# Kernel optimization log

Measured on AMD Instinct MI355X. Metric: run time of the kernel, lower is better.

## Reference

```python
import jax, jax.numpy as jnp
import numpy as np

B, H, W, C = 8, 64, 64, 384
HEADS, WS = 12, 14
KD = C // HEADS          # key_dim = 32
D = KD                    # attn_ratio = 1 -> d = key_dim
DH = D * HEADS            # = 384
HID = 4 * C               # mlp hidden = 1536
SCALE = KD ** -0.5
EPS = 1e-5
N = WS * WS               # 196 tokens per window


def _bias_idx():
    pts = [(i, j) for i in range(WS) for j in range(WS)]
    off, idxs = {}, []
    for p1 in pts:
        for p2 in pts:
            o = (abs(p1[0] - p2[0]), abs(p1[1] - p2[1]))
            if o not in off:
                off[o] = len(off)
            idxs.append(off[o])
    return np.asarray(idxs, np.int32).reshape(N, N), len(off)


def setup_inputs() -> dict:
    key = jax.random.key(0)
    ks = jax.random.split(key, 8)
    bias_idx_np, n_off = _bias_idx()  # n_off == 196 for a 14x14 window
    s = 0.02
    return {
        "x": jax.random.normal(ks[0], (B, H * W, C), jnp.float32),
        "ln_attn_w": jnp.ones((C,), jnp.float32),
        "ln_attn_b": jnp.zeros((C,), jnp.float32),
        "qkv_w": jax.random.normal(ks[1], (3 * DH, C), jnp.float32) * s,
        "qkv_b": jnp.zeros((3 * DH,), jnp.float32),
        "proj_w": jax.random.normal(ks[2], (C, DH), jnp.float32) * s,
        "proj_b": jnp.zeros((C,), jnp.float32),
        "attn_biases": jax.random.normal(ks[3], (HEADS, n_off), jnp.float32) * s,
        "conv_w": jax.random.normal(ks[4], (C, 1, 3, 3), jnp.float32) * s,  # depthwise OIHW
        "bn_w": jnp.ones((C,), jnp.float32),
        "bn_b": jnp.zeros((C,), jnp.float32),
        "bn_mean": jnp.zeros((C,), jnp.float32),
        "bn_var": jnp.ones((C,), jnp.float32),
        "ln_mlp_w": jnp.ones((C,), jnp.float32),
        "ln_mlp_b": jnp.zeros((C,), jnp.float32),
        "fc1_w": jax.random.normal(ks[5], (HID, C), jnp.float32) * s,
        "fc1_b": jnp.zeros((HID,), jnp.float32),
        "fc2_w": jax.random.normal(ks[6], (C, HID), jnp.float32) * s,
        "fc2_b": jnp.zeros((C,), jnp.float32),
        "bias_idx": jnp.asarray(bias_idx_np),
    }


def _ln(x, w, b):
    m = jnp.mean(x, -1, keepdims=True)
    v = jnp.mean((x - m) ** 2, -1, keepdims=True)
    return (x - m) * jax.lax.rsqrt(v + EPS) * w + b


def reference(x, ln_attn_w, ln_attn_b, qkv_w, qkv_b, proj_w, proj_b, attn_biases,
              conv_w, bn_w, bn_b, bn_mean, bn_var, ln_mlp_w, ln_mlp_b,
              fc1_w, fc1_b, fc2_w, fc2_b, bias_idx):
    L = H * W
    res = x
    # ---- window partition (pad 64 -> 70, 5x5 windows of 14x14) ----
    pad = (-H) % WS
    pH = H + pad
    n = pH // WS
    xw = x.reshape(B, H, W, C)
    xw = jnp.pad(xw, ((0, 0), (0, pad), (0, pad), (0, 0)))
    xw = xw.reshape(B, n, WS, n, WS, C).transpose(0, 1, 3, 2, 4, 5)
    xw = xw.reshape(B * n * n, N, C)
    # ---- attention with relative-position bias ----
    xn = _ln(xw, ln_attn_w, ln_attn_b)
    qkv = xn @ qkv_w.T + qkv_b                       # [Bw, N, 3*DH]
    qkv = qkv.reshape(-1, N, HEADS, 3 * KD)
    q, k, v = qkv[..., :KD], qkv[..., KD:2 * KD], qkv[..., 2 * KD:]
    bias = attn_biases[:, bias_idx]                  # [HEADS, N, N]
    attn = jnp.einsum('bnhd,bmhd->bhnm', q, k) * SCALE + bias[None]
    attn = jax.nn.softmax(attn, axis=-1)
    out = jnp.einsum('bhnm,bmhd->bnhd', attn, v).reshape(-1, N, DH)
    out = out @ proj_w.T + proj_b
    # ---- window reverse + crop + residual ----
    out = out.reshape(B, n, n, WS, WS, C).transpose(0, 1, 3, 2, 4, 5)
    out = out.reshape(B, pH, pH, C)[:, :H, :W]
    x = res + out.reshape(B, L, C)
    # ---- depthwise local conv + BN (eval mode) ----
    xc = x.reshape(B, H, W, C).transpose(0, 3, 1, 2)  # NCHW
    xc = jax.lax.conv_general_dilated(xc, conv_w, (1, 1), 'SAME',
                                      feature_group_count=C)
    inv = jax.lax.rsqrt(bn_var + 1e-5)
    xc = (xc - bn_mean[None, :, None, None]) * (inv * bn_w)[None, :, None, None] \
         + bn_b[None, :, None, None]
    x = xc.reshape(B, C, L).transpose(0, 2, 1)
    # ---- MLP (LN -> fc1 -> GELU(exact) -> fc2) + residual ----
    h = _ln(x, ln_mlp_w, ln_mlp_b)
    h = jax.nn.gelu(h @ fc1_w.T + fc1_b, approximate=False)
    h = h @ fc2_w.T + fc2_b
    return x + h
```

## Files before the change

### kernel.cpp

```cpp
#include <hip/hip_runtime.h>
#include <hip/hip_bf16.h>

#define DI __device__ __forceinline__

typedef __attribute__((ext_vector_type(8))) __bf16 bf16x8;
typedef __attribute__((ext_vector_type(4))) float f32x4;
typedef __attribute__((ext_vector_type(2))) float f32x2;
typedef __attribute__((ext_vector_type(8))) unsigned short us8;
typedef __attribute__((ext_vector_type(4))) unsigned short us4;

constexpr int CBATCH = 8;
constexpr int HW = 64;
constexpr int CDIM = 384;
constexpr int HEADS = 12;
constexpr int WS = 14;
constexpr int NTOK = 196;
constexpr int NWIN = 200;
constexpr int MV = 39200;
constexpr int MPAD = 39296;
constexpr int NQKV = 1152;
constexpr int HIDD = 1536;
constexpr int MMLP = 32768;
constexpr int NBIAS = 12 * 13 * 13 * 4 * 16 * 4;
constexpr int PLSTR = 228;
constexpr float SCALE = 0.17677669529663687f;

DI unsigned short f2bf(float f) { __bf16 b = (__bf16)f; return __builtin_bit_cast(unsigned short, b); }
DI float bf2f(unsigned short u) { unsigned x = (unsigned)u << 16; return __builtin_bit_cast(float, x); }
DI bf16x8 ldfrag(const unsigned short* p) { return __builtin_bit_cast(bf16x8, *(const us8*)p); }
DI f32x4 mfma16(bf16x8 a, bf16x8 b, f32x4 c) {
  return __builtin_amdgcn_mfma_f32_16x16x32_bf16(a, b, c, 0, 0, 0);
}
DI void async16(const void* g, void* l) {
  __builtin_amdgcn_global_load_lds((const __attribute__((address_space(1))) void*)g,
                                   (__attribute__((address_space(3))) void*)l, 16, 0, 0);
}
DI int vt_addr(int d, int t) {
  return d * 256 + (((t & ~7) ^ ((d & 7) << 3) ^ (((d >> 3) & 3) << 5)) | (t & 7));
}

__global__ __launch_bounds__(256) void k_cvt(const float* __restrict__ s,
                                             unsigned short* __restrict__ d, int n) {
  int i = blockIdx.x * 256 + threadIdx.x;
  if (i < n) d[i] = f2bf(s[i]);
}

__global__ __launch_bounds__(256) void k_bias2(const float* __restrict__ ab,
                                               const int* __restrict__ bidx,
                                               unsigned short* __restrict__ bt, int n_off) {
  int i = blockIdx.x * 256 + threadIdx.x;
  if (i >= NBIAS) return;
  int r = i & 3, l15 = (i >> 2) & 15, g = (i >> 6) & 3;
  int j = i >> 8;
  int kt = j % 13;
  int j2 = j / 13;
  int qt = j2 % 13;
  int h = j2 / 13;
  int q = qt * 16 + l15, k = kt * 16 + g * 4 + r;
  float v = 0.f;
  if (q < 196 && k < 196) v = ab[h * n_off + bidx[q * 196 + k]];
  bt[i] = f2bf(v);
}

template <int WIN>
__global__ __launch_bounds__(256) void k_ln(const float* __restrict__ src,
                                            const float* __restrict__ lw,
                                            const float* __restrict__ lb,
                                            unsigned short* __restrict__ dst) {
  const int row = blockIdx.x * 4 + (threadIdx.x >> 6);
  const int l = threadIdx.x & 63;
  const int c0 = l * 6;
  const float* p;
  bool valid;
  if (WIN) {
    int win = row / 196, t = row - win * 196;
    int b = win / 25, wi = win - b * 25;
    int wr = wi / 5, wc = wi - wr * 5;
    int hh = wr * 14 + t / 14, ww = wc * 14 + (t - (t / 14) * 14);
    valid = (row < MV) && (hh < HW) && (ww < HW);
    p = src + ((size_t)b * 4096 + hh * 64 + ww) * CDIM;
  } else {
    valid = true;
    p = src + (size_t)row * CDIM;
  }
  float v[6];
  if (valid) {
    f32x2 a = *(const f32x2*)(p + c0);
    f32x2 b2 = *(const f32x2*)(p + c0 + 2);
    f32x2 c2 = *(const f32x2*)(p + c0 + 4);
    v[0] = a.x; v[1] = a.y; v[2] = b2.x; v[3] = b2.y; v[4] = c2.x; v[5] = c2.y;
  } else {
#pragma unroll
    for (int k = 0; k < 6; ++k) v[k] = 0.f;
  }
  float s = 0.f, q = 0.f;
#pragma unroll
  for (int k = 0; k < 6; ++k) { s += v[k]; q += v[k] * v[k]; }
#pragma unroll
  for (int m = 1; m <= 32; m <<= 1) {
    s += __shfl_xor(s, m, 64);
    q += __shfl_xor(q, m, 64);
  }
  float mean = s * (1.0f / 384.0f);
  float var = q * (1.0f / 384.0f) - mean * mean;
  float rs = rsqrtf(var + 1e-5f);
#pragma unroll
  for (int k = 0; k < 6; ++k) {
    float y = (v[k] - mean) * rs * lw[c0 + k] + lb[c0 + k];
    dst[(size_t)row * CDIM + c0 + k] = f2bf(y);
  }
}

__global__ __launch_bounds__(256) void k_conv(const float* __restrict__ x1,
                                              const float* __restrict__ cw,
                                              const float* __restrict__ bw,
                                              const float* __restrict__ bb,
                                              const float* __restrict__ bm,
                                              const float* __restrict__ bv,
                                              float* __restrict__ x2) {
  int idx = blockIdx.x * 256 + threadIdx.x;
  int c = idx % 384;
  int x = (idx / 384) & 63;
  int b = idx / (384 * 64);
  const float* base = x1 + (size_t)b * 4096 * 384 + c;
  float w[9];
#pragma unroll
  for (int k = 0; k < 9; ++k) w[k] = cw[c * 9 + k];
  float sc = rsqrtf(bv[c] + 1e-5f) * bw[c];
  float sb = bb[c] - bm[c] * sc;
  float t0m = 0.f, t0c = 0.f, t0p = 0.f;
  float t1m, t1c, t1p, t2m, t2c, t2p;
  t1m = (x > 0) ? base[(x - 1) * 384] : 0.f;
  t1c = base[x * 384];
  t1p = (x < 63) ? base[(x + 1) * 384] : 0.f;
  for (int y = 0; y < 64; ++y) {
    if (y < 63) {
      int ro = (y + 1) * 64;
      t2m = (x > 0) ? base[(ro + x - 1) * 384] : 0.f;
      t2c = base[(ro + x) * 384];
      t2p = (x < 63) ? base[(ro + x + 1) * 384] : 0.f;
    } else { t2m = t2c = t2p = 0.f; }
    float o = w[0] * t0m + w[1] * t0c + w[2] * t0p +
              w[3] * t1m + w[4] * t1c + w[5] * t1p +
              w[6] * t2m + w[7] * t2c + w[8] * t2p;
    x2[((size_t)b * 4096 + y * 64 + x) * 384 + c] = o * sc + sb;
    t0m = t1m; t0c = t1c; t0p = t1p;
    t1m = t2m; t1c = t2c; t1p = t2p;
  }
}

__global__ __launch_bounds__(256, 3) void k_attn(const unsigned short* __restrict__ qkv,
                                                 const unsigned short* __restrict__ bias_t,
                                                 unsigned short* __restrict__ aout) {
  __shared__ unsigned short Vt[32 * 256];
  __shared__ unsigned short Pl[4][16 * PLSTR];
  const int bid = blockIdx.x;
  const int blk = (bid & 7) * 300 + (bid >> 3);
  const int win = blk / 12, h = blk - win * 12;
  const int tid = threadIdx.x;
  const int w = tid >> 6, l = tid & 63;
  const int l15 = l & 15, g = l >> 4;
  const unsigned short* qb = qkv + (size_t)win * 196 * 1152 + h * 96;

  for (int i = tid; i < 896; i += 256) {
    int t = i >> 2, d8 = (i & 3) << 3;
    us8 z = {0, 0, 0, 0, 0, 0, 0, 0};
    if (t < 196) z = *(const us8*)(qb + (size_t)t * 1152 + 64 + d8);
#pragma unroll
    for (int j = 0; j < 8; ++j) Vt[vt_addr(d8 + j, t)] = z[j];
  }
  for (int z = l; z < 16 * 20; z += 64) {
    int rr = z / 20, cc = 208 + (z - rr * 20);
    Pl[w][rr * PLSTR + cc] = 0;
  }
  __syncthreads();

  bf16x8 bkv[13];
#pragma unroll
  for (int kt = 0; kt < 13; ++kt)
    bkv[kt] = ldfrag(qb + (size_t)(kt * 16 + l15) * 1152 + 32 + g * 8);

  const unsigned short* bth = bias_t + (size_t)h * (13 * 13 * 4 * 16 * 4);
  unsigned short* plw = &Pl[w][0];
  for (int qt = w; qt < 13; qt += 4) {
    bf16x8 aq = ldfrag(qb + (size_t)(qt * 16 + l15) * 1152 + g * 8);
    us4 bv[13];
#pragma unroll
    for (int kt = 0; kt < 13; ++kt)
      bv[kt] = *(const us4*)(bth + (size_t)(((qt * 13 + kt) * 4 + g) * 16 + l15) * 4);

    float su = 0.f;
#pragma unroll
    for (int kt = 0; kt < 13; ++kt) {
      f32x4 zz = {0.f, 0.f, 0.f, 0.f};
      f32x4 s = mfma16(bkv[kt], aq, zz);
      us4 pk;
#pragma unroll
      for (int r = 0; r < 4; ++r) {
        float p = __expf(s[r] + bf2f(bv[kt][r]));
        if (kt == 12 && g != 0) p = 0.f;
        su += p;
        pk[r] = f2bf(p);
      }
      *(us4*)(plw + l15 * PLSTR + kt * 16 + g * 4) = pk;
    }
    su += __shfl_xor(su, 16, 64);
    su += __shfl_xor(su, 32, 64);
    asm volatile("s_waitcnt lgkmcnt(0)" ::: "memory");
    __builtin_amdgcn_sched_barrier(0);
    f32x4 o0 = {0.f, 0.f, 0.f, 0.f}, o1 = {0.f, 0.f, 0.f, 0.f};
#pragma unroll
    for (int kc = 0; kc < 7; ++kc) {
      int t0 = kc * 32 + g * 8;
      bf16x8 pa = ldfrag(plw + l15 * PLSTR + t0);
      bf16x8 b0 = ldfrag(&Vt[vt_addr(l15, t0)]);
      bf16x8 b1 = ldfrag(&Vt[vt_addr(16 + l15, t0)]);
      o0 = mfma16(pa, b0, o0);
      o1 = mfma16(pa, b1, o1);
    }
    float inv = 1.0f / su;
#pragma unroll
    for (int r = 0; r < 4; ++r) {
      int rw = qt * 16 + g * 4 + r;
      if (rw < 196) {
        size_t rb = ((size_t)win * 196 + rw) * 384 + h * 32;
        aout[rb + l15] = f2bf(o0[r] * inv);
        aout[rb + 16 + l15] = f2bf(o1[r] * inv);
      }
    }
  }
}

template <int MODE, int K>
__global__ __launch_bounds__(256) void k_gemm(const unsigned short* __restrict__ A,
                                              const unsigned short* __restrict__ B,
                                              const float* __restrict__ bias,
                                              const float* __restrict__ auxr,
                                              float* __restrict__ auxw,
                                              unsigned short* __restrict__ outb) {
  __shared__ unsigned short As[128 * 64];
  __shared__ unsigned short Bs[128 * 64];
  const int tid = threadIdx.x;
  const int w = tid >> 6, l = tid & 63;
  const int l15 = l & 15, g = l >> 4;
  const int wm = w >> 1, wn = w & 1;
  const int nwg = gridDim.x * gridDim.y;
  const int orig = blockIdx.y * gridDim.x + blockIdx.x;
  const int cq = nwg >> 3, cr = nwg & 7;
  const int xcd = orig & 7, cidx = orig >> 3;
  const int flat = (xcd < cr ? xcd * (cq + 1) : cr * (cq + 1) + (xcd - cr) * cq) + cidx;
  const int bx = flat % gridDim.x, by = flat / gridDim.x;
  const size_t arow0 = (size_t)bx * 128;
  const size_t brow0 = (size_t)by * 128;
  f32x4 acc[4][4] = {};
  for (int ks = 0; ks < K; ks += 64) {
    if (ks) __syncthreads();
#pragma unroll
    for (int it = 0; it < 4; ++it) {
      const int f = it * 256 + tid;
      const int r = f >> 3, c8 = (f & 7) << 3;
      const int c8s = c8 ^ ((r & 7) << 3);
      const int lb = (it * 256 + w * 64) * 8;
      async16(A + (arow0 + r) * K + ks + c8s, &As[lb]);
      async16(B + (brow0 + r) * K + ks + c8s, &Bs[lb]);
    }
    __syncthreads();
#pragma unroll
    for (int kk = 0; kk < 2; ++kk) {
      bf16x8 af[4], bfr[4];
#pragma unroll
      for (int i = 0; i < 4; ++i) {
        const int row = wm * 64 + i * 16 + l15;
        af[i] = ldfrag(&As[row * 64 + ((kk * 32 + g * 8) ^ ((row & 7) << 3))]);
      }
#pragma unroll
      for (int j = 0; j < 4; ++j) {
        const int row = wn * 64 + j * 16 + l15;
        bfr[j] = ldfrag(&Bs[row * 64 + ((kk * 32 + g * 8) ^ ((row & 7) << 3))]);
      }
#pragma unroll
      for (int i = 0; i < 4; ++i)
#pragma unroll
        for (int j = 0; j < 4; ++j)
          acc[i][j] = mfma16(af[i], bfr[j], acc[i][j]);
    }
  }
#pragma unroll
  for (int i = 0; i < 4; ++i) {
#pragma unroll
    for (int j = 0; j < 4; ++j) {
#pragma unroll
      for (int r = 0; r < 4; ++r) {
        const int row = (int)arow0 + wm * 64 + i * 16 + g * 4 + r;
        const int col = (int)brow0 + wn * 64 + j * 16 + l15;
        float v = acc[i][j][r] + bias[col];
        if (MODE == 0) {
          int ch = col % 96;
          float o = (ch < 32) ? v * SCALE : v;
          outb[(size_t)row * NQKV + col] = f2bf(o);
        } else if (MODE == 1) {
          if (row < MV) {
            int win = row / 196, t = row - win * 196;
            int b = win / 25, wi = win - b * 25;
            int wr = wi / 5, wc = wi - wr * 5;
            int hh = wr * 14 + t / 14, ww = wc * 14 + (t - (t / 14) * 14);
            if (hh < HW && ww < HW) {
              size_t di = ((size_t)b * 4096 + hh * 64 + ww) * 384 + col;
              auxw[di] = auxr[di] + v;
            }
          }
        } else if (MODE == 2) {
          float gl = 0.5f * v * (1.0f + erff(v * 0.7071067811865475f));
          outb[(size_t)row * HIDD + col] = f2bf(gl);
        } else {
          size_t di = (size_t)row * 384 + col;
          auxw[di] = auxr[di] + v;
        }
      }
    }
  }
}

extern "C" void kernel_launch(void* const* d_in, const int* in_sizes, int n_in,
                              void* d_out, int out_size, void* d_ws, size_t ws_size,
                              hipStream_t stream) {
  const float* x = (const float*)d_in[0];
  const float* ln_attn_w = (const float*)d_in[1];
  const float* ln_attn_b = (const float*)d_in[2];
  const float* qkv_w = (const float*)d_in[3];
  const float* qkv_b = (const float*)d_in[4];
  const float* proj_w = (const float*)d_in[5];
  const float* proj_b = (const float*)d_in[6];
  const float* attn_biases = (const float*)d_in[7];
  const float* conv_w = (const float*)d_in[8];
  const float* bn_w = (const float*)d_in[9];
  const float* bn_b = (const float*)d_in[10];
  const float* bn_mean = (const float*)d_in[11];
  const float* bn_var = (const float*)d_in[12];
  const float* ln_mlp_w = (const float*)d_in[13];
  const float* ln_mlp_b = (const float*)d_in[14];
  const float* fc1_w = (const float*)d_in[15];
  const float* fc1_b = (const float*)d_in[16];
  const float* fc2_w = (const float*)d_in[17];
  const float* fc2_b = (const float*)d_in[18];
  const int* bias_idx = (const int*)d_in[19];

  char* ws = (char*)d_ws;
  size_t off = 0;
  auto alloc = [&](size_t n) {
    void* p = ws + off;
    off = (off + n + 255) & ~(size_t)255;
    return p;
  };
  unsigned short* xn = (unsigned short*)alloc((size_t)MPAD * CDIM * 2);
  unsigned short* qkv = (unsigned short*)alloc((size_t)MMLP * HIDD * 2);
  unsigned short* attn = (unsigned short*)alloc((size_t)MMLP * CDIM * 4);
  float* x1 = (float*)alloc((size_t)MMLP * CDIM * 4);
  unsigned short* wq = (unsigned short*)alloc((size_t)NQKV * CDIM * 2);
  unsigned short* wp = (unsigned short*)alloc((size_t)CDIM * CDIM * 2);
  unsigned short* w1 = (unsigned short*)alloc((size_t)HIDD * CDIM * 2);
  unsigned short* w2 = (unsigned short*)alloc((size_t)CDIM * HIDD * 2);
  unsigned short* bias_t = (unsigned short*)alloc((size_t)NBIAS * 2);
  unsigned short* hbuf = qkv;
  float* x2 = (float*)attn;
  unsigned short* xln = xn;
  int n_off = in_sizes[7] / HEADS;

  dim3 B256(256);
  k_cvt<<<dim3((NQKV * CDIM + 255) / 256), B256, 0, stream>>>(qkv_w, wq, NQKV * CDIM);
  k_cvt<<<dim3((CDIM * CDIM + 255) / 256), B256, 0, stream>>>(proj_w, wp, CDIM * CDIM);
  k_cvt<<<dim3((HIDD * CDIM + 255) / 256), B256, 0, stream>>>(fc1_w, w1, HIDD * CDIM);
  k_cvt<<<dim3((CDIM * HIDD + 255) / 256), B256, 0, stream>>>(fc2_w, w2, CDIM * HIDD);
  k_bias2<<<dim3((NBIAS + 255) / 256), B256, 0, stream>>>(attn_biases, bias_idx, bias_t, n_off);
  k_ln<1><<<dim3(MPAD / 4), B256, 0, stream>>>(x, ln_attn_w, ln_attn_b, xn);
  k_gemm<0, CDIM><<<dim3(MPAD / 128, NQKV / 128), B256, 0, stream>>>(xn, wq, qkv_b, nullptr, nullptr, qkv);
  k_attn<<<dim3(NWIN * HEADS), B256, 0, stream>>>(qkv, bias_t, attn);
  k_gemm<1, CDIM><<<dim3(MPAD / 128, CDIM / 128), B256, 0, stream>>>(attn, wp, proj_b, x, x1, nullptr);
  k_conv<<<dim3(CBATCH * HW * CDIM / 256), B256, 0, stream>>>(x1, conv_w, bn_w, bn_b, bn_mean, bn_var, x2);
  k_ln<0><<<dim3(MMLP / 4), B256, 0, stream>>>(x2, ln_mlp_w, ln_mlp_b, xln);
  k_gemm<2, CDIM><<<dim3(MMLP / 128, HIDD / 128), B256, 0, stream>>>(xln, w1, fc1_b, nullptr, nullptr, hbuf);
  k_gemm<3, HIDD><<<dim3(MMLP / 128, CDIM / 128), B256, 0, stream>>>(hbuf, w2, fc2_b, x2, (float*)d_out, nullptr);
}
```

Baseline: 557.5 us.

## Double-buffer LDS tiles in GEMM to overlap async loads with MFMA

Shared-memory A/B tiles in the GEMM kernel become two buffers. The next K-slice is issued asynchronously into one buffer while MFMAs consume the other, with the loop unrolled by two K-steps. This is meant to hide global-to-LDS load latency and cut one barrier per K-step. It doubles LDS use per block to 64KB, which can lower occupancy, and the loop assumes an even number of K tiles.

```diff
diff --git a/kernel.cpp b/kernel.cpp
--- a/kernel.cpp
+++ b/kernel.cpp
@@ -238,8 +238,8 @@
                                               const float* __restrict__ auxr,
                                               float* __restrict__ auxw,
                                               unsigned short* __restrict__ outb) {
-  __shared__ unsigned short As[128 * 64];
-  __shared__ unsigned short Bs[128 * 64];
+  __shared__ unsigned short As[2][128 * 64];
+  __shared__ unsigned short Bs[2][128 * 64];
   const int tid = threadIdx.x;
   const int w = tid >> 6, l = tid & 63;
   const int l15 = l & 15, g = l >> 4;
@@ -253,30 +253,31 @@
   const size_t arow0 = (size_t)bx * 128;
   const size_t brow0 = (size_t)by * 128;
   f32x4 acc[4][4] = {};
-  for (int ks = 0; ks < K; ks += 64) {
-    if (ks) __syncthreads();
+
+  auto stage = [&](unsigned short* as, unsigned short* bs, int ks) {
 #pragma unroll
     for (int it = 0; it < 4; ++it) {
       const int f = it * 256 + tid;
       const int r = f >> 3, c8 = (f & 7) << 3;
       const int c8s = c8 ^ ((r & 7) << 3);
       const int lb = (it * 256 + w * 64) * 8;
-      async16(A + (arow0 + r) * K + ks + c8s, &As[lb]);
-      async16(B + (brow0 + r) * K + ks + c8s, &Bs[lb]);
-    }
-    __syncthreads();
+      async16(A + (arow0 + r) * K + ks + c8s, as + lb);
+      async16(B + (brow0 + r) * K + ks + c8s, bs + lb);
+    }
+  };
+  auto compute = [&](const unsigned short* as, const unsigned short* bs) {
 #pragma unroll
     for (int kk = 0; kk < 2; ++kk) {
       bf16x8 af[4], bfr[4];
 #pragma unroll
       for (int i = 0; i < 4; ++i) {
         const int row = wm * 64 + i * 16 + l15;
-        af[i] = ldfrag(&As[row * 64 + ((kk * 32 + g * 8) ^ ((row & 7) << 3))]);
+        af[i] = ldfrag(&as[row * 64 + ((kk * 32 + g * 8) ^ ((row & 7) << 3))]);
       }
 #pragma unroll
       for (int j = 0; j < 4; ++j) {
         const int row = wn * 64 + j * 16 + l15;
-        bfr[j] = ldfrag(&Bs[row * 64 + ((kk * 32 + g * 8) ^ ((row & 7) << 3))]);
+        bfr[j] = ldfrag(&bs[row * 64 + ((kk * 32 + g * 8) ^ ((row & 7) << 3))]);
       }
 #pragma unroll
       for (int i = 0; i < 4; ++i)
@@ -284,7 +285,24 @@
         for (int j = 0; j < 4; ++j)
           acc[i][j] = mfma16(af[i], bfr[j], acc[i][j]);
     }
-  }
+  };
+
+  constexpr int NT = K / 64;
+  stage(As[0], Bs[0], 0);
+  __syncthreads();
+  for (int t = 0; t < NT - 2; t += 2) {
+    stage(As[1], Bs[1], (t + 1) * 64);
+    compute(As[0], Bs[0]);
+    __syncthreads();
+    stage(As[0], Bs[0], (t + 2) * 64);
+    compute(As[1], Bs[1]);
+    __syncthreads();
+  }
+  stage(As[1], Bs[1], (NT - 1) * 64);
+  compute(As[0], Bs[0]);
+  __syncthreads();
+  compute(As[1], Bs[1]);
+
 #pragma unroll
   for (int i = 0; i < 4; ++i) {
 #pragma unroll
```

Result: slower. 588.1 us (+5.5%).
